# Kernel optimization log

Hardware: AMD Instinct MI355X
Metric: run time of the kernel (lower is better)

Reference implementation:

```python
import jax, jax.numpy as jnp
import numpy as np

N = 100000   # nodes
E = 3200000  # edges
F = 128      # input features
H1 = 128     # first_gcn_dimensions
H2 = 64      # second_gcn_dimensions
D1 = 64      # first_dense_neurons
D2 = 8       # second_dense_neurons
L = 10       # number_of_labels


def setup_inputs() -> dict:
    key = jax.random.key(0)
    ks = jax.random.split(key, 8)
    edges = jax.random.randint(ks[0], (2, E), 0, N)
    features = jax.random.normal(ks[1], (N, F), dtype=jnp.float32)
    s = lambda k, shape: jax.random.normal(k, shape, dtype=jnp.float32) * 0.05
    return dict(
        edges=edges, features=features,
        W1=s(ks[2], (F, H1)), b1=jnp.zeros((H1,), jnp.float32),
        W2=s(ks[3], (H1, H2)), b2=jnp.zeros((H2,), jnp.float32),
        Wf1=s(ks[4], (H2, D1)), bf1=jnp.zeros((D1,), jnp.float32),
        Wf2=s(ks[5], (D1, D2)), bf2=jnp.zeros((D2,), jnp.float32),
        Wl=s(ks[6], (H2 * D2, L)), bl=jnp.zeros((L,), jnp.float32),
    )


def gcn_conv(x, W, b, src, dst, n):
    # PyG GCNConv: x' = D^{-1/2} (A + I) D^{-1/2} (x W) + b  (self-loops already in src/dst)
    h = x @ W                                            # [N, out]
    deg = jax.ops.segment_sum(jnp.ones(dst.shape[0], x.dtype), dst, num_segments=n)
    dinv = jnp.where(deg > 0, jax.lax.rsqrt(deg), 0.0)   # deg^{-1/2}, 0 for isolated
    norm = dinv[src] * dinv[dst]                         # [E+N]
    agg = jax.ops.segment_sum(h[src] * norm[:, None], dst, num_segments=n)
    return agg + b


def reference(edges, features, W1, b1, W2, b2, Wf1, bf1, Wf2, bf2, Wl, bl):
    n = features.shape[0]
    loop = jnp.arange(n)
    src = jnp.concatenate([edges[0], loop])
    dst = jnp.concatenate([edges[1], loop])

    h1 = jax.nn.relu(gcn_conv(features, W1, b1, src, dst, n))  # [N, H1]
    h2 = gcn_conv(h1, W2, b2, src, dst, n)                     # [N, H2]

    a1 = jnp.tanh(h2 @ Wf1 + bf1)                              # [N, D1]
    att = jax.nn.softmax(a1 @ Wf2 + bf2, axis=0)               # softmax over nodes, [N, D2]

    graph_embedding = (att.T @ h2).reshape(1, -1)              # [1, D2*H2]
    P = att.T @ att - jnp.eye(att.shape[1], dtype=att.dtype)   # [D2, D2]
    penalty = jnp.sum(jnp.sqrt(jnp.sum(P * P, axis=1)))

    predictions = jax.nn.log_softmax(graph_embedding @ Wl + bl, axis=1)  # [1, L]
    return graph_embedding, penalty, predictions
```

## Files before the change

### kernel.cpp

```cpp
#include <hip/hip_runtime.h>
#include <hip/hip_bf16.h>
#include <math.h>

#define NNODES 100000
#define NEDGES 3200000
#define NBUK ((NNODES + 127) >> 7)
#define NCHUNK 256
#define EPC (NEDGES / NCHUNK)

typedef float floatx2 __attribute__((ext_vector_type(2)));
typedef float f32x4 __attribute__((ext_vector_type(4)));
typedef short bf16x8 __attribute__((ext_vector_type(8)));

__device__ __forceinline__ unsigned short f2bf(float x) {
    unsigned u = __float_as_uint(x);
    unsigned r = u + 0x7FFFu + ((u >> 16) & 1u);
    return (unsigned short)(r >> 16);
}

__device__ __forceinline__ void acc8_fp8(uint2 v, floatx2* a) {
    a[0] += __builtin_amdgcn_cvt_pk_f32_fp8(v.x, false);
    a[1] += __builtin_amdgcn_cvt_pk_f32_fp8(v.x, true);
    a[2] += __builtin_amdgcn_cvt_pk_f32_fp8(v.y, false);
    a[3] += __builtin_amdgcn_cvt_pk_f32_fp8(v.y, true);
}
__device__ __forceinline__ void acc4_fp8(unsigned v, floatx2* a) {
    a[0] += __builtin_amdgcn_cvt_pk_f32_fp8(v, false);
    a[1] += __builtin_amdgcn_cvt_pk_f32_fp8(v, true);
}

__global__ void prep_w_kernel(const float* __restrict__ W1, const float* __restrict__ W2,
                              unsigned short* __restrict__ Wt1, unsigned short* __restrict__ Wt2) {
    int i = blockIdx.x * 256 + threadIdx.x;
    if (i < 128 * 128) {
        int k = i >> 7, n = i & 127;
        Wt1[n * 128 + k] = f2bf(W1[i]);
    } else if (i < 128 * 128 + 128 * 64) {
        int j = i - 128 * 128;
        int k = j >> 6, n = j & 63;
        Wt2[n * 128 + k] = f2bf(W2[j]);
    }
}

__global__ __launch_bounds__(1024) void chunk_hist_kernel(const int* __restrict__ dst,
                                                          int* __restrict__ hist) {
    __shared__ int h[NBUK];
    int c = blockIdx.x, t = threadIdx.x;
    for (int i = t; i < NBUK; i += 1024) h[i] = 0;
    __syncthreads();
    const int4* d4 = (const int4*)(dst + c * EPC);
    for (int i = t; i < EPC / 4; i += 1024) {
        int4 d = d4[i];
        atomicAdd(&h[d.x >> 7], 1);
        atomicAdd(&h[d.y >> 7], 1);
        atomicAdd(&h[d.z >> 7], 1);
        atomicAdd(&h[d.w >> 7], 1);
    }
    __syncthreads();
    for (int i = t; i < NBUK; i += 1024)
        hist[c * NBUK + i] = h[i];
}

__global__ void col_scan_kernel(int* __restrict__ hist, int* __restrict__ btot) {
    int t = blockIdx.x * 256 + threadIdx.x;
    if (t >= NBUK) return;
    int run = 0;
    for (int c = 0; c < NCHUNK; c++) {
        int idx = c * NBUK + t;
        int v = hist[idx];
        hist[idx] = run;
        run += v;
    }
    btot[t] = run;
}

__global__ void bucket_scan_kernel(const int* __restrict__ btot, int* __restrict__ bstart,
                                   int* __restrict__ row_start, float* __restrict__ smalls) {
    __shared__ int s[1024];
    int t = threadIdx.x;
    if (t < 592) smalls[t] = 0.0f;
    int v = (t < NBUK) ? btot[t] : 0;
    s[t] = v;
    __syncthreads();
    for (int off = 1; off < 1024; off <<= 1) {
        int x = (t >= off) ? s[t - off] : 0;
        __syncthreads();
        s[t] += x;
        __syncthreads();
    }
    if (t < NBUK) bstart[t] = s[t] - v;
    if (t == 0) {
        bstart[NBUK] = NEDGES;
        row_start[NNODES] = NEDGES;
    }
}

__global__ __launch_bounds__(1024) void chunk_scatter_kernel(const int* __restrict__ src,
                                                             const int* __restrict__ dst,
                                                             const int* __restrict__ hist,
                                                             const int* __restrict__ bstart,
                                                             int* __restrict__ ebuk) {
    __shared__ int cur[NBUK];
    int c = blockIdx.x, t = threadIdx.x;
    for (int i = t; i < NBUK; i += 1024)
        cur[i] = bstart[i] + hist[c * NBUK + i];
    __syncthreads();
    const int4* s4 = (const int4*)(src + c * EPC);
    const int4* d4 = (const int4*)(dst + c * EPC);
    for (int i = t; i < EPC / 4; i += 1024) {
        int4 s = s4[i];
        int4 d = d4[i];
        int p0 = atomicAdd(&cur[d.x >> 7], 1);
        ebuk[p0] = s.x | ((d.x & 127) << 20);
        int p1 = atomicAdd(&cur[d.y >> 7], 1);
        ebuk[p1] = s.y | ((d.y & 127) << 20);
        int p2 = atomicAdd(&cur[d.z >> 7], 1);
        ebuk[p2] = s.z | ((d.z & 127) << 20);
        int p3 = atomicAdd(&cur[d.w >> 7], 1);
        ebuk[p3] = s.w | ((d.w & 127) << 20);
    }
}

__global__ __launch_bounds__(256) void build_kernel(const int* __restrict__ ebuk,
                                                    const int* __restrict__ bstart,
                                                    int* __restrict__ row_start,
                                                    float* __restrict__ dinv,
                                                    int* __restrict__ csr) {
    __shared__ int cnt[128];
    __shared__ int scn[128];
    __shared__ int cur[128];
    int b = blockIdx.x;
    int t = threadIdx.x;
    int s0 = bstart[b], s1 = bstart[b + 1];
    if (t < 128) cnt[t] = 0;
    __syncthreads();
    for (int i = s0 + t; i < s1; i += 256)
        atomicAdd(&cnt[(ebuk[i] >> 20) & 127], 1);
    __syncthreads();
    if (t < 128) scn[t] = cnt[t];
    __syncthreads();
#pragma unroll
    for (int off = 1; off < 128; off <<= 1) {
        int x = (t < 128 && t >= off) ? scn[t - off] : 0;
        __syncthreads();
        if (t < 128) scn[t] += x;
        __syncthreads();
    }
    int node = b * 128 + t;
    if (t < 128) {
        int rs = s0 + scn[t] - cnt[t];
        cur[t] = rs;
        if (node < NNODES) {
            row_start[node] = rs;
            dinv[node] = rsqrtf((float)cnt[t] + 1.0f);
        }
    }
    __syncthreads();
    for (int i = s0 + t; i < s1; i += 256) {
        int v = ebuk[i];
        int pos = atomicAdd(&cur[(v >> 20) & 127], 1);
        csr[pos] = v & 0xFFFFF;
    }
}

template <int KIN, int KOUT, bool ABF16>
__global__ __launch_bounds__(256) void gemm_mfma_kernel(const void* __restrict__ Av,
                                                        const unsigned short* __restrict__ Wt,
                                                        const float* __restrict__ rowscale,
                                                        unsigned char* __restrict__ stage) {
    constexpr int LDK = KIN + 8;
    constexpr int LDC = KOUT + 4;
    constexpr int SH_AB = (64 + KOUT) * LDK * 2;
    constexpr int SH_C  = 64 * LDC * 4;
    constexpr int SH = SH_AB > SH_C ? SH_AB : SH_C;
    __shared__ char shbuf[SH];
    unsigned short* As = (unsigned short*)shbuf;
    unsigned short* Ws = As + 64 * LDK;
    float* Cs = (float*)shbuf;
    int t = threadIdx.x;
    int block_row = blockIdx.x * 64;

    for (int idx = t; idx < KOUT * (KIN / 8); idx += 256) {
        int n = idx / (KIN / 8), c = idx % (KIN / 8);
        *(uint4*)(Ws + n * LDK + c * 8) = *(const uint4*)(Wt + n * KIN + c * 8);
    }
    if (ABF16) {
        const unsigned short* A = (const unsigned short*)Av;
        for (int idx = t; idx < 64 * (KIN / 8); idx += 256) {
            int r = idx / (KIN / 8), c = idx % (KIN / 8);
            uint4 v = make_uint4(0, 0, 0, 0);
            if (block_row + r < NNODES)
                v = *(const uint4*)(A + (size_t)(block_row + r) * KIN + c * 8);
            *(uint4*)(As + r * LDK + c * 8) = v;
        }
    } else {
        const float* A = (const float*)Av;
        for (int idx = t; idx < 64 * (KIN / 4); idx += 256) {
            int r = idx / (KIN / 4), c = idx % (KIN / 4);
            float4 v = make_float4(0.f, 0.f, 0.f, 0.f);
            if (block_row + r < NNODES)
                v = *(const float4*)(A + (size_t)(block_row + r) * KIN + c * 4);
            unsigned p0 = (unsigned)f2bf(v.x) | ((unsigned)f2bf(v.y) << 16);
            unsigned p1 = (unsigned)f2bf(v.z) | ((unsigned)f2bf(v.w) << 16);
            *(uint2*)(As + r * LDK + c * 4) = make_uint2(p0, p1);
        }
    }
    __syncthreads();

    int wv = t >> 6, lane = t & 63;
    int r0 = wv * 16;
    int m = lane & 15, q = lane >> 4;
    constexpr int NT = KOUT / 16;
    constexpr int KS = KIN / 32;
    f32x4 acc[NT];
#pragma unroll
    for (int nt = 0; nt < NT; nt++) acc[nt] = (f32x4)(0.f);
    bf16x8 afr[KS];
#pragma unroll
    for (int ks = 0; ks < KS; ks++)
        afr[ks] = *(bf16x8*)(As + (r0 + m) * LDK + ks * 32 + q * 8);
#pragma unroll
    for (int nt = 0; nt < NT; nt++) {
#pragma unroll
        for (int ks = 0; ks < KS; ks++) {
            bf16x8 b = *(bf16x8*)(Ws + (nt * 16 + m) * LDK + ks * 32 + q * 8);
            acc[nt] = __builtin_amdgcn_mfma_f32_16x16x32_bf16(afr[ks], b, acc[nt], 0, 0, 0);
        }
    }
    __syncthreads();
#pragma unroll
    for (int nt = 0; nt < NT; nt++)
#pragma unroll
        for (int j = 0; j < 4; j++)
            Cs[(r0 + q * 4 + j) * LDC + nt * 16 + m] = acc[nt][j];
    __syncthreads();
    for (int idx = t; idx < 64 * (KOUT / 4); idx += 256) {
        int r = idx / (KOUT / 4), c4 = idx % (KOUT / 4);
        int row = block_row + r;
        if (row < NNODES) {
            float4 v = *(float4*)(Cs + r * LDC + c4 * 4);
            float d = rowscale[row];
            int pk = __builtin_amdgcn_cvt_pk_fp8_f32(v.x * d, v.y * d, 0, false);
            pk = __builtin_amdgcn_cvt_pk_fp8_f32(v.z * d, v.w * d, pk, true);
            *(unsigned*)(stage + (size_t)row * KOUT + c4 * 4) = (unsigned)pk;
        }
    }
}

__global__ __launch_bounds__(256) void gather128_kernel(
    const unsigned char* __restrict__ hs, const int* __restrict__ row_start,
    const int* __restrict__ csr, const float* __restrict__ dinv,
    const float* __restrict__ bias, unsigned short* __restrict__ out) {
    int wave = threadIdx.x >> 6;
    int lane = threadIdx.x & 63;
    int n = blockIdx.x * 4 + wave;
    if (n >= NNODES) return;
    int g = lane >> 4;
    int c = lane & 15;
    unsigned boff = (unsigned)c << 3;
    int start = row_start[n], end = row_start[n + 1];
    floatx2 acc[4];
#pragma unroll
    for (int i = 0; i < 4; i++) acc[i] = (floatx2)(0.f);
    int w = (start + 3) & ~3;
    if (w > end) w = end;
    {
        int e2 = start + g;
        if (e2 < w) {
            unsigned o = ((unsigned)csr[e2] << 7) + boff;
            acc8_fp8(*(const uint2*)(hs + o), acc);
        }
    }
    for (; w + 32 <= end; w += 32) {
        int4 ca = *(const int4*)(csr + w + 4 * g);
        int4 cbv = *(const int4*)(csr + w + 16 + 4 * g);
        uint2 v0 = *(const uint2*)(hs + (((unsigned)ca.x  << 7) + boff));
        uint2 v1 = *(const uint2*)(hs + (((unsigned)ca.y  << 7) + boff));
        uint2 v2 = *(const uint2*)(hs + (((unsigned)ca.z  << 7) + boff));
        uint2 v3 = *(const uint2*)(hs + (((unsigned)ca.w  << 7) + boff));
        uint2 v4 = *(const uint2*)(hs + (((unsigned)cbv.x << 7) + boff));
        uint2 v5 = *(const uint2*)(hs + (((unsigned)cbv.y << 7) + boff));
        uint2 v6 = *(const uint2*)(hs + (((unsigned)cbv.z << 7) + boff));
        uint2 v7 = *(const uint2*)(hs + (((unsigned)cbv.w << 7) + boff));
        acc8_fp8(v0, acc); acc8_fp8(v1, acc); acc8_fp8(v2, acc); acc8_fp8(v3, acc);
        acc8_fp8(v4, acc); acc8_fp8(v5, acc); acc8_fp8(v6, acc); acc8_fp8(v7, acc);
    }
    for (; w + 16 <= end; w += 16) {
        int4 cs = *(const int4*)(csr + w + 4 * g);
        uint2 v0 = *(const uint2*)(hs + (((unsigned)cs.x << 7) + boff));
        uint2 v1 = *(const uint2*)(hs + (((unsigned)cs.y << 7) + boff));
        uint2 v2 = *(const uint2*)(hs + (((unsigned)cs.z << 7) + boff));
        uint2 v3 = *(const uint2*)(hs + (((unsigned)cs.w << 7) + boff));
        acc8_fp8(v0, acc); acc8_fp8(v1, acc); acc8_fp8(v2, acc); acc8_fp8(v3, acc);
    }
    for (int e2 = w + g; e2 < end; e2 += 4) {
        unsigned o = ((unsigned)csr[e2] << 7) + boff;
        acc8_fp8(*(const uint2*)(hs + o), acc);
    }
#pragma unroll
    for (int off = 16; off <= 32; off <<= 1)
#pragma unroll
        for (int i = 0; i < 4; i++) {
            acc[i].x += __shfl_xor(acc[i].x, off);
            acc[i].y += __shfl_xor(acc[i].y, off);
        }
    if (g == 0) {
        floatx2 s[4];
#pragma unroll
        for (int i = 0; i < 4; i++) s[i] = (floatx2)(0.f);
        acc8_fp8(*(const uint2*)(hs + (((unsigned)n << 7) + boff)), s);
        float d = dinv[n];
        int j = c * 8;
        float4 b0 = *(const float4*)(bias + j);
        float4 b1 = *(const float4*)(bias + j + 4);
        float r0 = fmaxf((acc[0].x + s[0].x) * d + b0.x, 0.f);
        float r1 = fmaxf((acc[0].y + s[0].y) * d + b0.y, 0.f);
        float r2 = fmaxf((acc[1].x + s[1].x) * d + b0.z, 0.f);
        float r3 = fmaxf((acc[1].y + s[1].y) * d + b0.w, 0.f);
        float r4 = fmaxf((acc[2].x + s[2].x) * d + b1.x, 0.f);
        float r5 = fmaxf((acc[2].y + s[2].y) * d + b1.y, 0.f);
        float r6 = fmaxf((acc[3].x + s[3].x) * d + b1.z, 0.f);
        float r7 = fmaxf((acc[3].y + s[3].y) * d + b1.w, 0.f);
        uint4 p;
        p.x = (unsigned)f2bf(r0) | ((unsigned)f2bf(r1) << 16);
        p.y = (unsigned)f2bf(r2) | ((unsigned)f2bf(r3) << 16);
        p.z = (unsigned)f2bf(r4) | ((unsigned)f2bf(r5) << 16);
        p.w = (unsigned)f2bf(r6) | ((unsigned)f2bf(r7) << 16);
        *(uint4*)(out + (((size_t)n << 7) + j)) = p;
    }
}

__global__ __launch_bounds__(256) void gather64_kernel(
    const unsigned char* __restrict__ hs, const int* __restrict__ row_start,
    const int* __restrict__ csr, const float* __restrict__ dinv,
    const float* __restrict__ bias, float* __restrict__ out) {
    int wave = threadIdx.x >> 6;
    int lane = threadIdx.x & 63;
    int n = blockIdx.x * 4 + wave;
    if (n >= NNODES) return;
    int g = lane >> 4;
    int c = lane & 15;
    unsigned boff = (unsigned)c << 2;
    int start = row_start[n], end = row_start[n + 1];
    floatx2 acc[2];
    acc[0] = (floatx2)(0.f); acc[1] = (floatx2)(0.f);
    int w = (start + 3) & ~3;
    if (w > end) w = end;
    {
        int e2 = start + g;
        if (e2 < w) {
            unsigned o = ((unsigned)csr[e2] << 6) + boff;
            acc4_fp8(*(const unsigned*)(hs + o), acc);
        }
    }
    for (; w + 32 <= end; w += 32) {
        int4 ca = *(const int4*)(csr + w + 4 * g);
        int4 cbv = *(const int4*)(csr + w + 16 + 4 * g);
        unsigned v0 = *(const unsigned*)(hs + (((unsigned)ca.x  << 6) + boff));
        unsigned v1 = *(const unsigned*)(hs + (((unsigned)ca.y  << 6) + boff));
        unsigned v2 = *(const unsigned*)(hs + (((unsigned)ca.z  << 6) + boff));
        unsigned v3 = *(const unsigned*)(hs + (((unsigned)ca.w  << 6) + boff));
        unsigned v4 = *(const unsigned*)(hs + (((unsigned)cbv.x << 6) + boff));
        unsigned v5 = *(const unsigned*)(hs + (((unsigned)cbv.y << 6) + boff));
        unsigned v6 = *(const unsigned*)(hs + (((unsigned)cbv.z << 6) + boff));
        unsigned v7 = *(const unsigned*)(hs + (((unsigned)cbv.w << 6) + boff));
        acc4_fp8(v0, acc); acc4_fp8(v1, acc); acc4_fp8(v2, acc); acc4_fp8(v3, acc);
        acc4_fp8(v4, acc); acc4_fp8(v5, acc); acc4_fp8(v6, acc); acc4_fp8(v7, acc);
    }
    for (; w + 16 <= end; w += 16) {
        int4 cs = *(const int4*)(csr + w + 4 * g);
        unsigned v0 = *(const unsigned*)(hs + (((unsigned)cs.x << 6) + boff));
        unsigned v1 = *(const unsigned*)(hs + (((unsigned)cs.y << 6) + boff));
        unsigned v2 = *(const unsigned*)(hs + (((unsigned)cs.z << 6) + boff));
        unsigned v3 = *(const unsigned*)(hs + (((unsigned)cs.w << 6) + boff));
        acc4_fp8(v0, acc); acc4_fp8(v1, acc); acc4_fp8(v2, acc); acc4_fp8(v3, acc);
    }
    for (int e2 = w + g; e2 < end; e2 += 4) {
        unsigned o = ((unsigned)csr[e2] << 6) + boff;
        acc4_fp8(*(const unsigned*)(hs + o), acc);
    }
#pragma unroll
    for (int off = 16; off <= 32; off <<= 1)
#pragma unroll
        for (int i = 0; i < 2; i++) {
            acc[i].x += __shfl_xor(acc[i].x, off);
            acc[i].y += __shfl_xor(acc[i].y, off);
        }
    if (g == 0) {
        floatx2 s[2];
        s[0] = (floatx2)(0.f); s[1] = (floatx2)(0.f);
        acc4_fp8(*(const unsigned*)(hs + (((unsigned)n << 6) + boff)), s);
        float d = dinv[n];
        int j = c * 4;
        float4 b4 = *(const float4*)(bias + j);
        float4 r;
        r.x = (acc[0].x + s[0].x) * d + b4.x;
        r.y = (acc[0].y + s[0].y) * d + b4.y;
        r.z = (acc[1].x + s[1].x) * d + b4.z;
        r.w = (acc[1].y + s[1].y) * d + b4.w;
        *(float4*)(out + (((size_t)n << 6) + j)) = r;
    }
}

__global__ __launch_bounds__(256) void attnpool_kernel(const float* __restrict__ h2,
                                                       const float* __restrict__ Wf1,
                                                       const float* __restrict__ bf1,
                                                       const float* __restrict__ Wf2,
                                                       const float* __restrict__ bf2,
                                                       float* __restrict__ ge,
                                                       float* __restrict__ ata,
                                                       float* __restrict__ colsum) {
    __shared__ float h2S[64][68];
    __shared__ float a1S[64][68];
    __shared__ float attS[64][8];
    __shared__ float colS[8][64];
    int t = threadIdx.x;
    int d0 = t >> 6;
    int j  = t & 63;
    int de = t >> 3, ee = t & 7;
    float accge0 = 0.f, accge1 = 0.f, accata = 0.f, acccol = 0.f;
    int ntiles = (NNODES + 63) / 64;
    for (int tile = blockIdx.x; tile < ntiles; tile += gridDim.x) {
        int base = tile * 64;
#pragma unroll
        for (int q = 0; q < 4; q++) {
            int idx = t + q * 256;
            int r = idx >> 4, cc = (idx & 15) * 4;
            int row = base + r;
            float4 v = (row < NNODES) ? *(const float4*)(h2 + (size_t)row * 64 + cc)
                                      : make_float4(0.f, 0.f, 0.f, 0.f);
            *(float4*)(&h2S[r][cc]) = v;
        }
        __syncthreads();
        {
            int cg = t & 15, rg = t >> 4;
            int jj = cg * 4, r0 = rg * 4;
            float4 b4 = *(const float4*)(bf1 + jj);
            float4 acc[4];
#pragma unroll
            for (int r = 0; r < 4; r++) acc[r] = b4;
#pragma unroll 4
            for (int k = 0; k < 64; k++) {
                float4 wv = *(const float4*)(Wf1 + (size_t)k * 64 + jj);
#pragma unroll
                for (int r = 0; r < 4; r++) {
                    float a = h2S[r0 + r][k];
                    acc[r].x += a * wv.x; acc[r].y += a * wv.y;
                    acc[r].z += a * wv.z; acc[r].w += a * wv.w;
                }
            }
#pragma unroll
            for (int r = 0; r < 4; r++) {
                a1S[r0 + r][jj]     = tanhf(acc[r].x);
                a1S[r0 + r][jj + 1] = tanhf(acc[r].y);
                a1S[r0 + r][jj + 2] = tanhf(acc[r].z);
                a1S[r0 + r][jj + 3] = tanhf(acc[r].w);
            }
        }
        __syncthreads();
        {
            int cc = t & 7, r = t >> 3;
#pragma unroll
            for (int h = 0; h < 2; h++) {
                int rr = r + h * 32;
                float acc = bf2[cc];
                for (int k = 0; k < 64; k++)
                    acc += a1S[rr][k] * Wf2[(size_t)k * 8 + cc];
                float ev = (base + rr < NNODES) ? __expf(acc) : 0.f;
                attS[rr][cc] = ev;
                colS[cc][rr] = ev;
            }
        }
        __syncthreads();
#pragma unroll 8
        for (int i = 0; i < 64; i++) {
            float hv = h2S[i][j];
            accge0 += attS[i][d0] * hv;
            accge1 += attS[i][d0 + 4] * hv;
        }
        if (t < 64) {
#pragma unroll 8
            for (int i = 0; i < 64; i++) accata += attS[i][de] * attS[i][ee];
        }
        if (t < 8) {
            float s = 0.f;
#pragma unroll
            for (int r = 0; r < 64; r++) s += colS[t][r];
            acccol += s;
        }
        __syncthreads();
    }
    atomicAdd(ge + d0 * 64 + j, accge0);
    atomicAdd(ge + (d0 + 4) * 64 + j, accge1);
    if (t < 64) atomicAdd(ata + de * 8 + ee, accata);
    if (t < 8) atomicAdd(colsum + t, acccol);
}

__global__ void final_kernel(const float* __restrict__ geacc, const float* __restrict__ ata,
                             const float* __restrict__ colsum, const float* __restrict__ Wl,
                             const float* __restrict__ bl, float* __restrict__ out) {
    __shared__ float geF[512];
    __shared__ float inv[8];
    __shared__ float logits[10];
    int t = threadIdx.x;
    if (t < 8) inv[t] = 1.0f / colsum[t];
    __syncthreads();
    for (int idx = t; idx < 512; idx += 64) {
        int d = idx >> 6;
        float v = geacc[idx] * inv[d];
        geF[idx] = v;
        out[idx] = v;
    }
    __syncthreads();
    if (t == 0) {
        float pen = 0.f;
        for (int d = 0; d < 8; d++) {
            float s = 0.f;
            for (int e = 0; e < 8; e++) {
                float p = ata[d * 8 + e] * inv[d] * inv[e] - (d == e ? 1.0f : 0.0f);
                s += p * p;
            }
            pen += sqrtf(s);
        }
        out[512] = pen;
    }
    if (t < 10) {
        float acc = bl[t];
        for (int k = 0; k < 512; k++) acc += geF[k] * Wl[(size_t)k * 10 + t];
        logits[t] = acc;
    }
    __syncthreads();
    if (t == 0) {
        float m = -INFINITY;
        for (int l = 0; l < 10; l++) m = fmaxf(m, logits[l]);
        float s = 0.f;
        for (int l = 0; l < 10; l++) s += expf(logits[l] - m);
        float ls = logf(s);
        for (int l = 0; l < 10; l++) out[513 + l] = logits[l] - m - ls;
    }
}

extern "C" void kernel_launch(void* const* d_in, const int* in_sizes, int n_in,
                              void* d_out, int out_size, void* d_ws, size_t ws_size,
                              hipStream_t stream) {
    const int* esrc = (const int*)d_in[0];
    const int* edst = esrc + NEDGES;
    const float* X   = (const float*)d_in[1];
    const float* W1  = (const float*)d_in[2];
    const float* b1  = (const float*)d_in[3];
    const float* W2  = (const float*)d_in[4];
    const float* b2  = (const float*)d_in[5];
    const float* Wf1 = (const float*)d_in[6];
    const float* bf1 = (const float*)d_in[7];
    const float* Wf2 = (const float*)d_in[8];
    const float* bf2 = (const float*)d_in[9];
    const float* Wl  = (const float*)d_in[10];
    const float* bl  = (const float*)d_in[11];
    float* out = (float*)d_out;

    float* ws     = (float*)d_ws;
    float* dinv   = ws;
    float* smalls = ws + 100352;
    float* colsum = smalls + 8;
    float* ata    = smalls + 16;
    float* geacc  = smalls + 80;
    float* A = ws + 101376;
    float* B = A + (size_t)NNODES * 128;
    int* row_start = (int*)(B + (size_t)NNODES * 128);
    int* btot      = row_start + 100352;
    int* bstart    = btot + 1024;
    int* csr       = bstart + 1024;
    unsigned short* Wt1 = (unsigned short*)(csr + NEDGES);
    unsigned short* Wt2 = Wt1 + 128 * 128;
    int* ebuk      = (int*)A;
    int* hist      = (int*)B;
    unsigned char* stage = (unsigned char*)A;
    unsigned short* h1 = (unsigned short*)B;
    float* h2  = B;

    prep_w_kernel<<<96, 256, 0, stream>>>(W1, W2, Wt1, Wt2);

    chunk_hist_kernel<<<NCHUNK, 1024, 0, stream>>>(edst, hist);
    col_scan_kernel<<<4, 256, 0, stream>>>(hist, btot);
    bucket_scan_kernel<<<1, 1024, 0, stream>>>(btot, bstart, row_start, smalls);
    chunk_scatter_kernel<<<NCHUNK, 1024, 0, stream>>>(esrc, edst, hist, bstart, ebuk);
    build_kernel<<<NBUK, 256, 0, stream>>>(ebuk, bstart, row_start, dinv, csr);

    gemm_mfma_kernel<128, 128, false><<<(NNODES + 63) / 64, 256, 0, stream>>>(X, Wt1, dinv, stage);
    gather128_kernel<<<(NNODES + 3) / 4, 256, 0, stream>>>(stage, row_start, csr, dinv, b1, h1);

    gemm_mfma_kernel<128, 64, true><<<(NNODES + 63) / 64, 256, 0, stream>>>(h1, Wt2, dinv, stage);
    gather64_kernel<<<(NNODES + 3) / 4, 256, 0, stream>>>(stage, row_start, csr, dinv, b2, h2);

    attnpool_kernel<<<512, 256, 0, stream>>>(h2, Wf1, bf1, Wf2, bf2, geacc, ata, colsum);
    final_kernel<<<1, 64, 0, stream>>>(geacc, ata, colsum, Wl, bl, out);
}
```

Baseline: 424.5 us.

## Slice fp8 feature staging into 32-byte column slices and parallelize column scan

The GEMM epilogue now writes the fp8 intermediate features as 32-byte column slices, one contiguous slab per slice. A single templated gather kernel replaces the 128- and 64-wide gathers: each block handles one slice for four nodes and spreads 16 edges across each wave, aiming for better cache locality and more memory parallelism per wave. The cost is that the CSR indices are re-read once per slice, and each feature access shrinks to 32 bytes. Separately, the per-bucket column scan over chunk histograms becomes a block-level shared-memory scan with one block per bucket, instead of 4 blocks each looping serially over 256 chunks.

New measurement: 542.5 us. +27.8%, slower.

```diff
diff --git a/kernel.cpp b/kernel.cpp
--- a/kernel.cpp
+++ b/kernel.cpp
@@ -8,6 +8,8 @@
 #define NCHUNK 256
 #define EPC (NEDGES / NCHUNK)
 
+#define SLICE_BYTES ((size_t)100352 * 32)
+
 typedef float floatx2 __attribute__((ext_vector_type(2)));
 typedef float f32x4 __attribute__((ext_vector_type(4)));
 typedef short bf16x8 __attribute__((ext_vector_type(8)));
@@ -23,10 +25,6 @@
     a[1] += __builtin_amdgcn_cvt_pk_f32_fp8(v.x, true);
     a[2] += __builtin_amdgcn_cvt_pk_f32_fp8(v.y, false);
     a[3] += __builtin_amdgcn_cvt_pk_f32_fp8(v.y, true);
-}
-__device__ __forceinline__ void acc4_fp8(unsigned v, floatx2* a) {
-    a[0] += __builtin_amdgcn_cvt_pk_f32_fp8(v, false);
-    a[1] += __builtin_amdgcn_cvt_pk_f32_fp8(v, true);
 }
 
 __global__ void prep_w_kernel(const float* __restrict__ W1, const float* __restrict__ W2,
@@ -61,17 +59,23 @@
         hist[c * NBUK + i] = h[i];
 }
 
-__global__ void col_scan_kernel(int* __restrict__ hist, int* __restrict__ btot) {
-    int t = blockIdx.x * 256 + threadIdx.x;
-    if (t >= NBUK) return;
-    int run = 0;
-    for (int c = 0; c < NCHUNK; c++) {
-        int idx = c * NBUK + t;
-        int v = hist[idx];
-        hist[idx] = run;
-        run += v;
-    }
-    btot[t] = run;
+__global__ __launch_bounds__(256) void col_scan_kernel(int* __restrict__ hist,
+                                                       int* __restrict__ btot) {
+    __shared__ int sdat[NCHUNK];
+    int b = blockIdx.x;
+    int t = threadIdx.x;
+    int v = hist[t * NBUK + b];
+    sdat[t] = v;
+    __syncthreads();
+#pragma unroll
+    for (int off = 1; off < NCHUNK; off <<= 1) {
+        int x = (t >= off) ? sdat[t - off] : 0;
+        __syncthreads();
+        sdat[t] += x;
+        __syncthreads();
+    }
+    hist[t * NBUK + b] = sdat[t] - v;
+    if (t == NCHUNK - 1) btot[b] = sdat[t];
 }
 
 __global__ void bucket_scan_kernel(const int* __restrict__ btot, int* __restrict__ bstart,
@@ -242,163 +246,91 @@
             float d = rowscale[row];
             int pk = __builtin_amdgcn_cvt_pk_fp8_f32(v.x * d, v.y * d, 0, false);
             pk = __builtin_amdgcn_cvt_pk_fp8_f32(v.z * d, v.w * d, pk, true);
-            *(unsigned*)(stage + (size_t)row * KOUT + c4 * 4) = (unsigned)pk;
-        }
-    }
-}
-
-__global__ __launch_bounds__(256) void gather128_kernel(
+            *(unsigned*)(stage + (size_t)(c4 >> 3) * SLICE_BYTES
+                               + ((size_t)row << 5) + ((c4 & 7) << 2)) = (unsigned)pk;
+        }
+    }
+}
+
+template <int S, bool L1OUT>
+__global__ __launch_bounds__(256) void gather_sliced_kernel(
     const unsigned char* __restrict__ hs, const int* __restrict__ row_start,
     const int* __restrict__ csr, const float* __restrict__ dinv,
-    const float* __restrict__ bias, unsigned short* __restrict__ out) {
+    const float* __restrict__ bias, void* __restrict__ outv) {
+    constexpr int LOG2S = (S == 4) ? 2 : 1;
     int wave = threadIdx.x >> 6;
     int lane = threadIdx.x & 63;
-    int n = blockIdx.x * 4 + wave;
+    unsigned b = blockIdx.x;
+    int s = (int)(b & (S - 1));
+    int n = (int)((b >> LOG2S) << 2) + wave;
     if (n >= NNODES) return;
-    int g = lane >> 4;
-    int c = lane & 15;
+    int eg = lane >> 2;
+    int c = lane & 3;
+    const unsigned char* hss = hs + (size_t)s * SLICE_BYTES;
     unsigned boff = (unsigned)c << 3;
     int start = row_start[n], end = row_start[n + 1];
     floatx2 acc[4];
 #pragma unroll
     for (int i = 0; i < 4; i++) acc[i] = (floatx2)(0.f);
-    int w = (start + 3) & ~3;
+    int w = (start + 1) & ~1;
     if (w > end) w = end;
-    {
-        int e2 = start + g;
-        if (e2 < w) {
-            unsigned o = ((unsigned)csr[e2] << 7) + boff;
-            acc8_fp8(*(const uint2*)(hs + o), acc);
-        }
+    if (start + eg < w) {
+        unsigned o = ((unsigned)csr[start] << 5) + boff;
+        acc8_fp8(*(const uint2*)(hss + o), acc);
     }
     for (; w + 32 <= end; w += 32) {
-        int4 ca = *(const int4*)(csr + w + 4 * g);
-        int4 cbv = *(const int4*)(csr + w + 16 + 4 * g);
-        uint2 v0 = *(const uint2*)(hs + (((unsigned)ca.x  << 7) + boff));
-        uint2 v1 = *(const uint2*)(hs + (((unsigned)ca.y  << 7) + boff));
-        uint2 v2 = *(const uint2*)(hs + (((unsigned)ca.z  << 7) + boff));
-        uint2 v3 = *(const uint2*)(hs + (((unsigned)ca.w  << 7) + boff));
-        uint2 v4 = *(const uint2*)(hs + (((unsigned)cbv.x << 7) + boff));
-        uint2 v5 = *(const uint2*)(hs + (((unsigned)cbv.y << 7) + boff));
-        uint2 v6 = *(const uint2*)(hs + (((unsigned)cbv.z << 7) + boff));
-        uint2 v7 = *(const uint2*)(hs + (((unsigned)cbv.w << 7) + boff));
-        acc8_fp8(v0, acc); acc8_fp8(v1, acc); acc8_fp8(v2, acc); acc8_fp8(v3, acc);
-        acc8_fp8(v4, acc); acc8_fp8(v5, acc); acc8_fp8(v6, acc); acc8_fp8(v7, acc);
-    }
-    for (; w + 16 <= end; w += 16) {
-        int4 cs = *(const int4*)(csr + w + 4 * g);
-        uint2 v0 = *(const uint2*)(hs + (((unsigned)cs.x << 7) + boff));
-        uint2 v1 = *(const uint2*)(hs + (((unsigned)cs.y << 7) + boff));
-        uint2 v2 = *(const uint2*)(hs + (((unsigned)cs.z << 7) + boff));
-        uint2 v3 = *(const uint2*)(hs + (((unsigned)cs.w << 7) + boff));
-        acc8_fp8(v0, acc); acc8_fp8(v1, acc); acc8_fp8(v2, acc); acc8_fp8(v3, acc);
-    }
-    for (int e2 = w + g; e2 < end; e2 += 4) {
-        unsigned o = ((unsigned)csr[e2] << 7) + boff;
-        acc8_fp8(*(const uint2*)(hs + o), acc);
-    }
-#pragma unroll
-    for (int off = 16; off <= 32; off <<= 1)
+        int2 cs = *(const int2*)(csr + w + 2 * eg);
+        uint2 v0 = *(const uint2*)(hss + (((unsigned)cs.x << 5) + boff));
+        uint2 v1 = *(const uint2*)(hss + (((unsigned)cs.y << 5) + boff));
+        acc8_fp8(v0, acc);
+        acc8_fp8(v1, acc);
+    }
+    for (int e2 = w + eg; e2 < end; e2 += 16) {
+        unsigned o = ((unsigned)csr[e2] << 5) + boff;
+        acc8_fp8(*(const uint2*)(hss + o), acc);
+    }
+#pragma unroll
+    for (int off = 4; off <= 32; off <<= 1)
 #pragma unroll
         for (int i = 0; i < 4; i++) {
             acc[i].x += __shfl_xor(acc[i].x, off);
             acc[i].y += __shfl_xor(acc[i].y, off);
         }
-    if (g == 0) {
-        floatx2 s[4];
-#pragma unroll
-        for (int i = 0; i < 4; i++) s[i] = (floatx2)(0.f);
-        acc8_fp8(*(const uint2*)(hs + (((unsigned)n << 7) + boff)), s);
+    if (eg == 0) {
+        floatx2 sf[4];
+#pragma unroll
+        for (int i = 0; i < 4; i++) sf[i] = (floatx2)(0.f);
+        acc8_fp8(*(const uint2*)(hss + (((unsigned)n << 5) + boff)), sf);
         float d = dinv[n];
-        int j = c * 8;
+        int j = s * 32 + c * 8;
         float4 b0 = *(const float4*)(bias + j);
         float4 b1 = *(const float4*)(bias + j + 4);
-        float r0 = fmaxf((acc[0].x + s[0].x) * d + b0.x, 0.f);
-        float r1 = fmaxf((acc[0].y + s[0].y) * d + b0.y, 0.f);
-        float r2 = fmaxf((acc[1].x + s[1].x) * d + b0.z, 0.f);
-        float r3 = fmaxf((acc[1].y + s[1].y) * d + b0.w, 0.f);
-        float r4 = fmaxf((acc[2].x + s[2].x) * d + b1.x, 0.f);
-        float r5 = fmaxf((acc[2].y + s[2].y) * d + b1.y, 0.f);
-        float r6 = fmaxf((acc[3].x + s[3].x) * d + b1.z, 0.f);
-        float r7 = fmaxf((acc[3].y + s[3].y) * d + b1.w, 0.f);
-        uint4 p;
-        p.x = (unsigned)f2bf(r0) | ((unsigned)f2bf(r1) << 16);
-        p.y = (unsigned)f2bf(r2) | ((unsigned)f2bf(r3) << 16);
-        p.z = (unsigned)f2bf(r4) | ((unsigned)f2bf(r5) << 16);
-        p.w = (unsigned)f2bf(r6) | ((unsigned)f2bf(r7) << 16);
-        *(uint4*)(out + (((size_t)n << 7) + j)) = p;
-    }
-}
-
-__global__ __launch_bounds__(256) void gather64_kernel(
-    const unsigned char* __restrict__ hs, const int* __restrict__ row_start,
-    const int* __restrict__ csr, const float* __restrict__ dinv,
-    const float* __restrict__ bias, float* __restrict__ out) {
-    int wave = threadIdx.x >> 6;
-    int lane = threadIdx.x & 63;
-    int n = blockIdx.x * 4 + wave;
-    if (n >= NNODES) return;
-    int g = lane >> 4;
-    int c = lane & 15;
-    unsigned boff = (unsigned)c << 2;
-    int start = row_start[n], end = row_start[n + 1];
-    floatx2 acc[2];
-    acc[0] = (floatx2)(0.f); acc[1] = (floatx2)(0.f);
-    int w = (start + 3) & ~3;
-    if (w > end) w = end;
-    {
-        int e2 = start + g;
-        if (e2 < w) {
-            unsigned o = ((unsigned)csr[e2] << 6) + boff;
-            acc4_fp8(*(const unsigned*)(hs + o), acc);
-        }
-    }
-    for (; w + 32 <= end; w += 32) {
-        int4 ca = *(const int4*)(csr + w + 4 * g);
-        int4 cbv = *(const int4*)(csr + w + 16 + 4 * g);
-        unsigned v0 = *(const unsigned*)(hs + (((unsigned)ca.x  << 6) + boff));
-        unsigned v1 = *(const unsigned*)(hs + (((unsigned)ca.y  << 6) + boff));
-        unsigned v2 = *(const unsigned*)(hs + (((unsigned)ca.z  << 6) + boff));
-        unsigned v3 = *(const unsigned*)(hs + (((unsigned)ca.w  << 6) + boff));
-        unsigned v4 = *(const unsigned*)(hs + (((unsigned)cbv.x << 6) + boff));
-        unsigned v5 = *(const unsigned*)(hs + (((unsigned)cbv.y << 6) + boff));
-        unsigned v6 = *(const unsigned*)(hs + (((unsigned)cbv.z << 6) + boff));
-        unsigned v7 = *(const unsigned*)(hs + (((unsigned)cbv.w << 6) + boff));
-        acc4_fp8(v0, acc); acc4_fp8(v1, acc); acc4_fp8(v2, acc); acc4_fp8(v3, acc);
-        acc4_fp8(v4, acc); acc4_fp8(v5, acc); acc4_fp8(v6, acc); acc4_fp8(v7, acc);
-    }
-    for (; w + 16 <= end; w += 16) {
-        int4 cs = *(const int4*)(csr + w + 4 * g);
-        unsigned v0 = *(const unsigned*)(hs + (((unsigned)cs.x << 6) + boff));
-        unsigned v1 = *(const unsigned*)(hs + (((unsigned)cs.y << 6) + boff));
-        unsigned v2 = *(const unsigned*)(hs + (((unsigned)cs.z << 6) + boff));
-        unsigned v3 = *(const unsigned*)(hs + (((unsigned)cs.w << 6) + boff));
-        acc4_fp8(v0, acc); acc4_fp8(v1, acc); acc4_fp8(v2, acc); acc4_fp8(v3, acc);
-    }
-    for (int e2 = w + g; e2 < end; e2 += 4) {
-        unsigned o = ((unsigned)csr[e2] << 6) + boff;
-        acc4_fp8(*(const unsigned*)(hs + o), acc);
-    }
-#pragma unroll
-    for (int off = 16; off <= 32; off <<= 1)
-#pragma unroll
-        for (int i = 0; i < 2; i++) {
-            acc[i].x += __shfl_xor(acc[i].x, off);
-            acc[i].y += __shfl_xor(acc[i].y, off);
-        }
-    if (g == 0) {
-        floatx2 s[2];
-        s[0] = (floatx2)(0.f); s[1] = (floatx2)(0.f);
-        acc4_fp8(*(const unsigned*)(hs + (((unsigned)n << 6) + boff)), s);
-        float d = dinv[n];
-        int j = c * 4;
-        float4 b4 = *(const float4*)(bias + j);
-        float4 r;
-        r.x = (acc[0].x + s[0].x) * d + b4.x;
-        r.y = (acc[0].y + s[0].y) * d + b4.y;
-        r.z = (acc[1].x + s[1].x) * d + b4.z;
-        r.w = (acc[1].y + s[1].y) * d + b4.w;
-        *(float4*)(out + (((size_t)n << 6) + j)) = r;
+        float r0 = (acc[0].x + sf[0].x) * d + b0.x;
+        float r1 = (acc[0].y + sf[0].y) * d + b0.y;
+        float r2 = (acc[1].x + sf[1].x) * d + b0.z;
+        float r3 = (acc[1].y + sf[1].y) * d + b0.w;
+        float r4 = (acc[2].x + sf[2].x) * d + b1.x;
+        float r5 = (acc[2].y + sf[2].y) * d + b1.y;
+        float r6 = (acc[3].x + sf[3].x) * d + b1.z;
+        float r7 = (acc[3].y + sf[3].y) * d + b1.w;
+        if (L1OUT) {
+            r0 = fmaxf(r0, 0.f); r1 = fmaxf(r1, 0.f);
+            r2 = fmaxf(r2, 0.f); r3 = fmaxf(r3, 0.f);
+            r4 = fmaxf(r4, 0.f); r5 = fmaxf(r5, 0.f);
+            r6 = fmaxf(r6, 0.f); r7 = fmaxf(r7, 0.f);
+            uint4 p;
+            p.x = (unsigned)f2bf(r0) | ((unsigned)f2bf(r1) << 16);
+            p.y = (unsigned)f2bf(r2) | ((unsigned)f2bf(r3) << 16);
+            p.z = (unsigned)f2bf(r4) | ((unsigned)f2bf(r5) << 16);
+            p.w = (unsigned)f2bf(r6) | ((unsigned)f2bf(r7) << 16);
+            *(uint4*)((unsigned short*)outv + (((size_t)n << 7) + j)) = p;
+        } else {
+            float4 o0 = make_float4(r0, r1, r2, r3);
+            float4 o1 = make_float4(r4, r5, r6, r7);
+            float* op = (float*)outv + (((size_t)n << 6) + j);
+            *(float4*)op = o0;
+            *(float4*)(op + 4) = o1;
+        }
     }
 }
 
@@ -581,16 +513,16 @@
     prep_w_kernel<<<96, 256, 0, stream>>>(W1, W2, Wt1, Wt2);
 
     chunk_hist_kernel<<<NCHUNK, 1024, 0, stream>>>(edst, hist);
-    col_scan_kernel<<<4, 256, 0, stream>>>(hist, btot);
+    col_scan_kernel<<<NBUK, 256, 0, stream>>>(hist, btot);
     bucket_scan_kernel<<<1, 1024, 0, stream>>>(btot, bstart, row_start, smalls);
     chunk_scatter_kernel<<<NCHUNK, 1024, 0, stream>>>(esrc, edst, hist, bstart, ebuk);
     build_kernel<<<NBUK, 256, 0, stream>>>(ebuk, bstart, row_start, dinv, csr);
 
     gemm_mfma_kernel<128, 128, false><<<(NNODES + 63) / 64, 256, 0, stream>>>(X, Wt1, dinv, stage);
-    gather128_kernel<<<(NNODES + 3) / 4, 256, 0, stream>>>(stage, row_start, csr, dinv, b1, h1);
+    gather_sliced_kernel<4, true><<<(NNODES / 4) * 4, 256, 0, stream>>>(stage, row_start, csr, dinv, b1, h1);
 
     gemm_mfma_kernel<128, 64, true><<<(NNODES + 63) / 64, 256, 0, stream>>>(h1, Wt2, dinv, stage);
-    gather64_kernel<<<(NNODES + 3) / 4, 256, 0, stream>>>(stage, row_start, csr, dinv, b2, h2);
+    gather_sliced_kernel<2, false><<<(NNODES / 4) * 2, 256, 0, stream>>>(stage, row_start, csr, dinv, b2, h2);
 
     attnpool_kernel<<<512, 256, 0, stream>>>(h2, Wf1, bf1, Wf2, bf2, geacc, ata, colsum);
     final_kernel<<<1, 64, 0, stream>>>(geacc, ata, colsum, Wl, bl, out);
```
